# Performance work log

Hardware: AMD Instinct MI355X
Metric: run time of the kernel (lower is better)

## Reference

```python
import jax, jax.numpy as jnp
import numpy as np

B, N, D = 16384, 32, 256
J, P = 23, 2  # num_joints, dim_per_out_node


def setup_inputs() -> dict:
    key = jax.random.key(0)
    k1, k2, k3 = jax.random.split(key, 3)
    x = jax.random.normal(k1, (B, N, D), dtype=jnp.float32)
    # per-joint Linear params: weight [J, P, D] (torch Linear layout), bias [J, P]
    W = jax.random.normal(k2, (J, P, D), dtype=jnp.float32) * (1.0 / np.sqrt(D))
    b = jax.random.normal(k3, (J, P), dtype=jnp.float32) * 0.01
    # node_for_joint[j] = index of the node mapped to joint j (here nodes 0..22)
    node_for_joint = jnp.arange(J, dtype=jnp.int32)
    return {"x": x, "W": W, "b": b, "node_for_joint": node_for_joint}


def reference(x, W, b, node_for_joint):
    # Gather the node embedding feeding each joint: [B, J, D]
    xj = x[:, node_for_joint, :]
    # Apply each joint's distinct tiny Linear head as one batched contraction.
    # out[b, j, p] = sum_d xj[b, j, d] * W[j, p, d] + b[j, p]
    out = jnp.einsum("bjd,jpd->bjp", xj, W) + b  # [B, J, P]
    return out
```

## Files before the change

kernel.cpp:

```cpp
#include <hip/hip_runtime.h>


constexpr int Bn = 16384;
constexpr int Nn = 32;
constexpr int Dn = 256;
constexpr int Jn = 23;
constexpr int Pn = 2;

__global__ __launch_bounds__(256) void detok_kernel(
    const float* __restrict__ x, const float* __restrict__ W,
    const float* __restrict__ bias, const int* __restrict__ nfj,
    float* __restrict__ out)
{
    const int tid   = blockIdx.x * blockDim.x + threadIdx.x;
    const int wave  = tid >> 6;
    const int lane  = threadIdx.x & 63;
    const int group = lane >> 4;
    const int gl    = lane & 15;

    const int pair = wave * 4 + group;
    const int b = pair / Jn;
    const int j = pair - b * Jn;
    const int node = nfj[j];

    const float4* __restrict__ xr =
        reinterpret_cast<const float4*>(x + ((size_t)b * Nn + node) * Dn);
    const float4* __restrict__ w0 =
        reinterpret_cast<const float4*>(W + ((size_t)j * Pn + 0) * Dn);
    const float4* __restrict__ w1 =
        reinterpret_cast<const float4*>(W + ((size_t)j * Pn + 1) * Dn);

    float s0 = 0.f, s1 = 0.f;
#pragma unroll
    for (int k = 0; k < 4; ++k) {
        const int idx = k * 16 + gl;
        float4 xv = xr[idx];
        float4 a0 = w0[idx];
        float4 a1 = w1[idx];
        s0 += xv.x * a0.x + xv.y * a0.y + xv.z * a0.z + xv.w * a0.w;
        s1 += xv.x * a1.x + xv.y * a1.y + xv.z * a1.z + xv.w * a1.w;
    }

#pragma unroll
    for (int off = 8; off >= 1; off >>= 1) {
        s0 += __shfl_xor(s0, off, 64);
        s1 += __shfl_xor(s1, off, 64);
    }

    if (gl == 0) {
        float2 bj = *reinterpret_cast<const float2*>(bias + j * Pn);
        float2 o;
        o.x = s0 + bj.x;
        o.y = s1 + bj.y;
        *reinterpret_cast<float2*>(out + (size_t)pair * Pn) = o;
    }
}

extern "C" void kernel_launch(void* const* d_in, const int* in_sizes, int n_in,
                              void* d_out, int out_size, void* d_ws, size_t ws_size,
                              hipStream_t stream) {
    const float* x    = (const float*)d_in[0];
    const float* W    = (const float*)d_in[1];
    const float* bias = (const float*)d_in[2];
    const int*   nfj  = (const int*)d_in[3];
    float* out = (float*)d_out;

    const int total_pairs = Bn * Jn;
    const int pairs_per_block = (256 / 64) * 4;
    const int grid = total_pairs / pairs_per_block;

    detok_kernel<<<grid, 256, 0, stream>>>(x, W, bias, nfj, out);
}
```

Before: 641.9 us.

## Assign each block one joint and a strip of rows, keeping weights in registers

The grid becomes 2D: blockIdx.y selects the joint and blockIdx.x a strip of 256 batch rows. Each wave loads that joint's two weight rows into registers once and loops over 64 rows, instead of reloading W for every (b,j) pair. x rows are read with nontemporal loads, and the shuffle width is narrowed to 16. Each block now reads far-apart 1KB rows strided across the batch, which may hurt DRAM locality, and the grid is much smaller (64x23 blocks), which limits parallelism for hiding memory latency.

New measurement: 626.0 us, median of 2. 2.5% less time.

```diff
diff --git a/kernel.cpp b/kernel.cpp
--- a/kernel.cpp
+++ b/kernel.cpp
@@ -7,52 +7,67 @@
 constexpr int Jn = 23;
 constexpr int Pn = 2;
 
+constexpr int ROWS_PER_BLOCK = 256;
+constexpr int WAVES_PER_BLOCK = 4;
+constexpr int ROWS_PER_WAVE = ROWS_PER_BLOCK / WAVES_PER_BLOCK;
+
+typedef float floatx4 __attribute__((ext_vector_type(4)));
+
 __global__ __launch_bounds__(256) void detok_kernel(
     const float* __restrict__ x, const float* __restrict__ W,
     const float* __restrict__ bias, const int* __restrict__ nfj,
     float* __restrict__ out)
 {
-    const int tid   = blockIdx.x * blockDim.x + threadIdx.x;
-    const int wave  = tid >> 6;
+    const int j     = blockIdx.y;
+    const int strip = blockIdx.x;
+    const int wave  = threadIdx.x >> 6;
     const int lane  = threadIdx.x & 63;
     const int group = lane >> 4;
     const int gl    = lane & 15;
 
-    const int pair = wave * 4 + group;
-    const int b = pair / Jn;
-    const int j = pair - b * Jn;
     const int node = nfj[j];
 
-    const float4* __restrict__ xr =
-        reinterpret_cast<const float4*>(x + ((size_t)b * Nn + node) * Dn);
-    const float4* __restrict__ w0 =
-        reinterpret_cast<const float4*>(W + ((size_t)j * Pn + 0) * Dn);
-    const float4* __restrict__ w1 =
-        reinterpret_cast<const float4*>(W + ((size_t)j * Pn + 1) * Dn);
-
-    float s0 = 0.f, s1 = 0.f;
+    const floatx4* __restrict__ w0p =
+        reinterpret_cast<const floatx4*>(W + ((size_t)j * Pn + 0) * Dn);
+    const floatx4* __restrict__ w1p =
+        reinterpret_cast<const floatx4*>(W + ((size_t)j * Pn + 1) * Dn);
+    floatx4 w0[4], w1[4];
 #pragma unroll
     for (int k = 0; k < 4; ++k) {
-        const int idx = k * 16 + gl;
-        float4 xv = xr[idx];
-        float4 a0 = w0[idx];
-        float4 a1 = w1[idx];
-        s0 += xv.x * a0.x + xv.y * a0.y + xv.z * a0.z + xv.w * a0.w;
-        s1 += xv.x * a1.x + xv.y * a1.y + xv.z * a1.z + xv.w * a1.w;
+        w0[k] = w0p[k * 16 + gl];
+        w1[k] = w1p[k * 16 + gl];
     }
 
+    const float2 bj = *reinterpret_cast<const float2*>(bias + j * Pn);
+
+    const int b0 = strip * ROWS_PER_BLOCK + wave * ROWS_PER_WAVE;
+
+#pragma unroll 2
+    for (int it = 0; it < ROWS_PER_WAVE; it += 4) {
+        const int b = b0 + it + group;
+        const floatx4* __restrict__ xr = reinterpret_cast<const floatx4*>(
+            x + ((size_t)b * Nn + node) * Dn);
+
+        float s0 = 0.f, s1 = 0.f;
 #pragma unroll
-    for (int off = 8; off >= 1; off >>= 1) {
-        s0 += __shfl_xor(s0, off, 64);
-        s1 += __shfl_xor(s1, off, 64);
-    }
+        for (int k = 0; k < 4; ++k) {
+            floatx4 xv = __builtin_nontemporal_load(&xr[k * 16 + gl]);
+            s0 += xv.x * w0[k].x + xv.y * w0[k].y + xv.z * w0[k].z + xv.w * w0[k].w;
+            s1 += xv.x * w1[k].x + xv.y * w1[k].y + xv.z * w1[k].z + xv.w * w1[k].w;
+        }
 
-    if (gl == 0) {
-        float2 bj = *reinterpret_cast<const float2*>(bias + j * Pn);
-        float2 o;
-        o.x = s0 + bj.x;
-        o.y = s1 + bj.y;
-        *reinterpret_cast<float2*>(out + (size_t)pair * Pn) = o;
+#pragma unroll
+        for (int off = 8; off >= 1; off >>= 1) {
+            s0 += __shfl_xor(s0, off, 16);
+            s1 += __shfl_xor(s1, off, 16);
+        }
+
+        if (gl == 0) {
+            float2 o;
+            o.x = s0 + bj.x;
+            o.y = s1 + bj.y;
+            *reinterpret_cast<float2*>(out + ((size_t)b * Jn + j) * Pn) = o;
+        }
     }
 }
 
@@ -65,9 +80,6 @@
     const int*   nfj  = (const int*)d_in[3];
     float* out = (float*)d_out;
 
-    const int total_pairs = Bn * Jn;
-    const int pairs_per_block = (256 / 64) * 4;
-    const int grid = total_pairs / pairs_per_block;
-
+    dim3 grid(Bn / ROWS_PER_BLOCK, Jn);
     detok_kernel<<<grid, 256, 0, stream>>>(x, W, bias, nfj, out);
 }
```
